# Kernel tuning notes

Hardware: AMD Instinct MI355X
Metric: run time of the kernel (lower is better)

## Reference

```python
import jax, jax.numpy as jnp
import numpy as np

BL = 5
N = 2 ** BL  # 32; LUT is (N+1) x (N+1)


def setup_inputs() -> dict:
    key = jax.random.key(0)
    k1, k2, k3 = jax.random.split(key, 3)
    M, K, O = 512, 256, 256
    x = jax.random.uniform(k1, (M, K), dtype=jnp.float32)              # activations in [0,1)
    W = jax.random.uniform(k2, (O, K), dtype=jnp.float32) * 2.0 - 1.0  # weights in [-1,1)
    b = jax.random.uniform(k3, (O,), dtype=jnp.float32) * 2.0 - 1.0
    # Stochastic-computing multiplication LUT: A[i, j] ~ i*j/N (floored), i,j in [0, N]
    i = np.arange(N + 1, dtype=np.float32)
    lut = jnp.asarray(np.floor(np.outer(i, i) / N), dtype=jnp.float32)
    return {"x": x, "W": W, "b": b, "lut": lut}


def _sanitize(t):
    t = jnp.where(jnp.isnan(t), jnp.zeros_like(t), t)
    return jnp.where(jnp.isinf(t), jnp.ones_like(t), t)


def sc_mat_mac_p(a, b, c, lut, n):
    # Faithful port of SC_MAT_MAC_p: quantize -> LUT gather over all (row, out) pairs ->
    # sign-correct -> reduce over K -> requantize -> add quantized bias -> rescale.
    a = _sanitize(a)
    b = _sanitize(b)
    c = _sanitize(c)
    amax = jnp.abs(a).max()
    amax = jnp.where(amax == 0, jnp.ones_like(amax), amax)
    dmax = jnp.maximum(jnp.abs(b).max(), jnp.abs(c).max())
    dmax = jnp.where(dmax == 0, jnp.ones_like(dmax), dmax)
    # SBL2 = int(log2(int(N / amax))); SN2 = 2**SBL2 (truncations match torch int())
    sn2 = 2.0 ** jnp.floor(jnp.log2(jnp.floor(n / amax)))
    sn1 = 2.0 ** jnp.floor(jnp.log2(jnp.floor(n / dmax)))
    aa = (a * sn2).astype(jnp.int32)  # [M, K], |aa| <= N
    bb = (b * sn1).astype(jnp.int32)  # [O, K], |bb| <= N
    cc = (c * sn1).astype(jnp.int32)  # [O]
    # LUT gather over the full cross product (original materializes this via
    # repeat_interleave/repeat; here it is a broadcasted gather of shape [M, O, K]).
    prod = lut[jnp.abs(aa)[:, None, :], jnp.abs(bb)[None, :, :]]          # [M, O, K]
    sgn = (jnp.sign(aa)[:, None, :] * jnp.sign(bb)[None, :, :]).astype(prod.dtype)
    x9 = (sgn * prod).sum(axis=-1)                                        # [M, O]
    d = (x9 / sn2).astype(jnp.int32) + cc[None, :]
    return d.astype(jnp.float32) / sn1


def reference(x, W, b, lut):
    # out = linear(x); out.data = SC_MAT_MAC_p(...)  -> value is the SC result,
    # gradient path is the dense linear (straight-through via .data assignment).
    lin = x @ W.T + b
    p = sc_mat_mac_p(x, W, b, lut, N)
    return lin + jax.lax.stop_gradient(p - lin)
```

## Files before the change

### kernel.cpp

```cpp
#include <hip/hip_runtime.h>
#include <stdint.h>


#define MROWS 512
#define KDIM  256
#define OCOLS 256

__device__ __forceinline__ void get_scales(float amax, float dmax, int& e2, int& e1) {
    if (amax == 0.0f) amax = 1.0f;
    if (dmax == 0.0f) dmax = 1.0f;
    float q2 = 32.0f / amax;
    float q1 = 32.0f / dmax;
    int f2 = (q2 >= 1073741824.0f) ? 0x40000000 : (int)floorf(q2);
    int f1 = (q1 >= 1073741824.0f) ? 0x40000000 : (int)floorf(q1);
    if (f2 < 1) f2 = 1;
    if (f1 < 1) f1 = 1;
    e2 = 31 - __clz(f2);
    e1 = 31 - __clz(f1);
}

__device__ __forceinline__ float max4(float4 v) {
    return fmaxf(fmaxf(fabsf(v.x), fabsf(v.y)), fmaxf(fabsf(v.z), fabsf(v.w)));
}

__device__ __forceinline__ int mac_loop(const float* __restrict__ W, int o,
                                        const unsigned int* a_sh, float sn1f) {
    const float4* wrow = (const float4*)(W + (size_t)o * KDIM);
    int sum = 0;
    #pragma unroll 8
    for (int kk = 0; kk < KDIM / 4; ++kk) {
        float4 wv = wrow[kk];
        unsigned int ap = a_sh[kk];
        float wfv[4] = {wv.x, wv.y, wv.z, wv.w};
        #pragma unroll
        for (int j = 0; j < 4; ++j) {
            int bv = (int)(wfv[j] * sn1f);
            int av = ((int)(ap << (24 - 8 * j))) >> 24;
            int s  = av * bv;
            sum += (s + ((s >> 31) & 31)) >> 5;
        }
    }
    return sum;
}

__global__ __launch_bounds__(256)
void k_scales(unsigned int* __restrict__ wsp, const float* __restrict__ x,
              const float* __restrict__ W, const float* __restrict__ b) {
    __shared__ float sm[8];
    const int m = blockIdx.x;
    const int o = threadIdx.x;
    const int wave = o >> 6;

    const float4* xf = (const float4*)x;
    const float4* wf = (const float4*)W;
    float va = fmaxf(max4(xf[m * 512 + o]), max4(xf[m * 512 + 256 + o]));
    float vd = max4(wf[m * 256 + o]);
    if (m == 0 && o < 64)
        vd = fmaxf(vd, max4(((const float4*)b)[o]));
    #pragma unroll
    for (int s = 32; s >= 1; s >>= 1) {
        va = fmaxf(va, __shfl_xor(va, s, 64));
        vd = fmaxf(vd, __shfl_xor(vd, s, 64));
    }
    if ((o & 63) == 0) { sm[2 * wave] = va; sm[2 * wave + 1] = vd; }
    __syncthreads();
    if (o == 0) {
        float a = fmaxf(fmaxf(sm[0], sm[2]), fmaxf(sm[4], sm[6]));
        float d = fmaxf(fmaxf(sm[1], sm[3]), fmaxf(sm[5], sm[7]));
        wsp[2 * m]     = __float_as_uint(a);
        wsp[2 * m + 1] = __float_as_uint(d);
    }
}

__global__ __launch_bounds__(256)
void k_main(const unsigned int* __restrict__ wsp, const float* __restrict__ x,
            const float* __restrict__ W, const float* __restrict__ b,
            float* __restrict__ out) {
    __shared__ unsigned int a_sh[KDIM / 4];
    __shared__ int s_e[2];

    const int m = blockIdx.x;
    const int o = threadIdx.x;

    float bo = b[o];
    float4 xv;
    if (o < KDIM / 4)
        xv = ((const float4*)(x + (size_t)m * KDIM))[o];

    if (o < 64) {
        float va = __uint_as_float(wsp[2 * o]);
        float vd = __uint_as_float(wsp[2 * o + 1]);
        #pragma unroll
        for (int s = 32; s >= 1; s >>= 1) {
            va = fmaxf(va, __shfl_xor(va, s, 64));
            vd = fmaxf(vd, __shfl_xor(vd, s, 64));
        }
        if (o == 0) {
            int e2, e1;
            get_scales(va, vd, e2, e1);
            s_e[0] = e2; s_e[1] = e1;
        }
    }
    __syncthreads();

    const int e2 = s_e[0];
    const int e1 = s_e[1];
    const float sn2f = (float)(1 << e2);
    const float sn1f = (float)(1 << e1);

    if (o < KDIM / 4) {
        int a0 = (int)(xv.x * sn2f) & 0xFF;
        int a1 = (int)(xv.y * sn2f) & 0xFF;
        int a2 = (int)(xv.z * sn2f) & 0xFF;
        int a3 = (int)(xv.w * sn2f) & 0xFF;
        a_sh[o] = (unsigned int)(a0 | (a1 << 8) | (a2 << 16) | (a3 << 24));
    }
    __syncthreads();

    int sum = mac_loop(W, o, a_sh, sn1f);

    int cc = (int)(bo * sn1f);
    int d  = ((sum + ((sum >> 31) & ((1 << e2) - 1))) >> e2) + cc;
    out[(size_t)m * OCOLS + o] = (float)d * (1.0f / sn1f);
}

extern "C" void kernel_launch(void* const* d_in, const int* in_sizes, int n_in,
                              void* d_out, int out_size, void* d_ws, size_t ws_size,
                              hipStream_t stream) {
    const float* x = (const float*)d_in[0];
    const float* W = (const float*)d_in[1];
    const float* b = (const float*)d_in[2];
    float* out = (float*)d_out;
    unsigned int* wsp = (unsigned int*)d_ws;

    k_scales<<<64,    256, 0, stream>>>(wsp, x, W, b);
    k_main  <<<MROWS, 256, 0, stream>>>(wsp, x, W, b, out);
}
```

Measured before the change: 76.77 us.

## Fuse scale reduction into main kernel with redundant per-block global max

Merges the separate scale-reduction kernel into the main kernel. Each block now recomputes the global max of x, W and b by reading all of them (about 768 KB per block, served from L2), which removes one kernel launch and the round trip through workspace. Each block also handles two rows with 512 threads, halving the grid to 256 blocks and reusing each W load pattern across both rows. The cost is redundant L2 traffic for the reduction in every block.

```diff
diff --git a/kernel.cpp b/kernel.cpp
--- a/kernel.cpp
+++ b/kernel.cpp
@@ -5,6 +5,9 @@
 #define MROWS 512
 #define KDIM  256
 #define OCOLS 256
+#define NTHR  512
+#define RPB   2
+#define NBLK  (MROWS / RPB)
 
 __device__ __forceinline__ void get_scales(float amax, float dmax, int& e2, int& e1) {
     if (amax == 0.0f) amax = 1.0f;
@@ -23,14 +26,74 @@
     return fmaxf(fmaxf(fabsf(v.x), fabsf(v.y)), fmaxf(fabsf(v.z), fabsf(v.w)));
 }
 
-__device__ __forceinline__ int mac_loop(const float* __restrict__ W, int o,
-                                        const unsigned int* a_sh, float sn1f) {
+__global__ __launch_bounds__(NTHR)
+void k_fused(const float* __restrict__ x, const float* __restrict__ W,
+             const float* __restrict__ b, float* __restrict__ out) {
+    __shared__ unsigned int a_sh[RPB][KDIM / 4];
+    __shared__ float sm[2 * (NTHR / 64)];
+    __shared__ int s_e[2];
+
+    const int tid  = threadIdx.x;
+    const int wave = tid >> 6;
+    const int m0   = blockIdx.x * RPB;
+
+    const float4* xf = (const float4*)x;
+    const float4* wf = (const float4*)W;
+    float va = 0.0f, vd = 0.0f;
+    #pragma unroll 8
+    for (int i = 0; i < 32768 / NTHR; ++i)
+        va = fmaxf(va, max4(xf[i * NTHR + tid]));
+    #pragma unroll 8
+    for (int i = 0; i < 16384 / NTHR; ++i)
+        vd = fmaxf(vd, max4(wf[i * NTHR + tid]));
+    if (tid < 64)
+        vd = fmaxf(vd, max4(((const float4*)b)[tid]));
+    #pragma unroll
+    for (int s = 32; s >= 1; s >>= 1) {
+        va = fmaxf(va, __shfl_xor(va, s, 64));
+        vd = fmaxf(vd, __shfl_xor(vd, s, 64));
+    }
+    if ((tid & 63) == 0) { sm[2 * wave] = va; sm[2 * wave + 1] = vd; }
+    __syncthreads();
+    if (tid == 0) {
+        float a = sm[0], d = sm[1];
+        #pragma unroll
+        for (int i = 1; i < NTHR / 64; ++i) {
+            a = fmaxf(a, sm[2 * i]);
+            d = fmaxf(d, sm[2 * i + 1]);
+        }
+        int e2, e1;
+        get_scales(a, d, e2, e1);
+        s_e[0] = e2; s_e[1] = e1;
+    }
+    __syncthreads();
+
+    const int e2 = s_e[0];
+    const int e1 = s_e[1];
+    const float sn2f = (float)(1 << e2);
+    const float sn1f = (float)(1 << e1);
+
+    if (tid < RPB * (KDIM / 4)) {
+        const int r = tid >> 6;
+        const int o = tid & 63;
+        float4 xv = xf[(size_t)(m0 + r) * (KDIM / 4) + o];
+        int a0 = (int)(xv.x * sn2f) & 0xFF;
+        int a1 = (int)(xv.y * sn2f) & 0xFF;
+        int a2 = (int)(xv.z * sn2f) & 0xFF;
+        int a3 = (int)(xv.w * sn2f) & 0xFF;
+        a_sh[r][o] = (unsigned int)(a0 | (a1 << 8) | (a2 << 16) | (a3 << 24));
+    }
+    __syncthreads();
+
+    const int o = tid & (OCOLS - 1);
+    const int r = tid >> 8;
     const float4* wrow = (const float4*)(W + (size_t)o * KDIM);
+    const unsigned int* arow = a_sh[r];
     int sum = 0;
     #pragma unroll 8
     for (int kk = 0; kk < KDIM / 4; ++kk) {
         float4 wv = wrow[kk];
-        unsigned int ap = a_sh[kk];
+        unsigned int ap = arow[kk];
         float wfv[4] = {wv.x, wv.y, wv.z, wv.w};
         #pragma unroll
         for (int j = 0; j < 4; ++j) {
@@ -40,88 +103,10 @@
             sum += (s + ((s >> 31) & 31)) >> 5;
         }
     }
-    return sum;
-}
 
-__global__ __launch_bounds__(256)
-void k_scales(unsigned int* __restrict__ wsp, const float* __restrict__ x,
-              const float* __restrict__ W, const float* __restrict__ b) {
-    __shared__ float sm[8];
-    const int m = blockIdx.x;
-    const int o = threadIdx.x;
-    const int wave = o >> 6;
-
-    const float4* xf = (const float4*)x;
-    const float4* wf = (const float4*)W;
-    float va = fmaxf(max4(xf[m * 512 + o]), max4(xf[m * 512 + 256 + o]));
-    float vd = max4(wf[m * 256 + o]);
-    if (m == 0 && o < 64)
-        vd = fmaxf(vd, max4(((const float4*)b)[o]));
-    #pragma unroll
-    for (int s = 32; s >= 1; s >>= 1) {
-        va = fmaxf(va, __shfl_xor(va, s, 64));
-        vd = fmaxf(vd, __shfl_xor(vd, s, 64));
-    }
-    if ((o & 63) == 0) { sm[2 * wave] = va; sm[2 * wave + 1] = vd; }
-    __syncthreads();
-    if (o == 0) {
-        float a = fmaxf(fmaxf(sm[0], sm[2]), fmaxf(sm[4], sm[6]));
-        float d = fmaxf(fmaxf(sm[1], sm[3]), fmaxf(sm[5], sm[7]));
-        wsp[2 * m]     = __float_as_uint(a);
-        wsp[2 * m + 1] = __float_as_uint(d);
-    }
-}
-
-__global__ __launch_bounds__(256)
-void k_main(const unsigned int* __restrict__ wsp, const float* __restrict__ x,
-            const float* __restrict__ W, const float* __restrict__ b,
-            float* __restrict__ out) {
-    __shared__ unsigned int a_sh[KDIM / 4];
-    __shared__ int s_e[2];
-
-    const int m = blockIdx.x;
-    const int o = threadIdx.x;
-
-    float bo = b[o];
-    float4 xv;
-    if (o < KDIM / 4)
-        xv = ((const float4*)(x + (size_t)m * KDIM))[o];
-
-    if (o < 64) {
-        float va = __uint_as_float(wsp[2 * o]);
-        float vd = __uint_as_float(wsp[2 * o + 1]);
-        #pragma unroll
-        for (int s = 32; s >= 1; s >>= 1) {
-            va = fmaxf(va, __shfl_xor(va, s, 64));
-            vd = fmaxf(vd, __shfl_xor(vd, s, 64));
-        }
-        if (o == 0) {
-            int e2, e1;
-            get_scales(va, vd, e2, e1);
-            s_e[0] = e2; s_e[1] = e1;
-        }
-    }
-    __syncthreads();
-
-    const int e2 = s_e[0];
-    const int e1 = s_e[1];
-    const float sn2f = (float)(1 << e2);
-    const float sn1f = (float)(1 << e1);
-
-    if (o < KDIM / 4) {
-        int a0 = (int)(xv.x * sn2f) & 0xFF;
-        int a1 = (int)(xv.y * sn2f) & 0xFF;
-        int a2 = (int)(xv.z * sn2f) & 0xFF;
-        int a3 = (int)(xv.w * sn2f) & 0xFF;
-        a_sh[o] = (unsigned int)(a0 | (a1 << 8) | (a2 << 16) | (a3 << 24));
-    }
-    __syncthreads();
-
-    int sum = mac_loop(W, o, a_sh, sn1f);
-
-    int cc = (int)(bo * sn1f);
-    int d  = ((sum + ((sum >> 31) & ((1 << e2) - 1))) >> e2) + cc;
-    out[(size_t)m * OCOLS + o] = (float)d * (1.0f / sn1f);
+    const int cc = (int)(b[o] * sn1f);
+    const int d  = ((sum + ((sum >> 31) & ((1 << e2) - 1))) >> e2) + cc;
+    out[(size_t)(m0 + r) * OCOLS + o] = (float)d * (1.0f / sn1f);
 }
 
 extern "C" void kernel_launch(void* const* d_in, const int* in_sizes, int n_in,
@@ -131,8 +116,7 @@
     const float* W = (const float*)d_in[1];
     const float* b = (const float*)d_in[2];
     float* out = (float*)d_out;
-    unsigned int* wsp = (unsigned int*)d_ws;
+    (void)d_ws; (void)ws_size;
 
-    k_scales<<<64,    256, 0, stream>>>(wsp, x, W, b);
-    k_main  <<<MROWS, 256, 0, stream>>>(wsp, x, W, b, out);
+    k_fused<<<NBLK, NTHR, 0, stream>>>(x, W, b, out);
 }
```

Measured after the change: 94.34 us. 1.23x slower.
